# Performance work log

Hardware: AMD Instinct MI355X
Metric: run time of the kernel (lower is better)

## Reference

```python
import jax, jax.numpy as jnp
import numpy as np

CP_LEN = 256
FFT_SIZE = 1024
OFFSET = CP_LEN // 2                      # 128
PILOT_SPACING = 100
NSYMS = 824
TOTAL_SYMS = NSYMS + 1 + NSYMS // PILOT_SPACING   # 833
PAD_L = (FFT_SIZE - TOTAL_SYMS) // 2      # 95
PAD_R = FFT_SIZE - PAD_L - TOTAL_SYMS     # 96
PILOTS_IDX = np.arange(PAD_L, FFT_SIZE - PAD_R, PILOT_SPACING)  # 9 pilots

def _data_indices():
    # Statically unroll the original while-loop: gather all non-pilot data bins.
    idxs = []
    idx = 0
    jj = PAD_L + 1
    while idx < NSYMS:
        n = min(PILOT_SPACING - 1, NSYMS - idx)
        idxs.extend(range(jj, jj + n))
        idx += n
        jj += n + 1
    return np.asarray(idxs, dtype=np.int32)

DATA_IDX = _data_indices()  # [824]


def setup_inputs() -> dict:
    key = jax.random.key(0)
    # [batch, n_symbols, 2*(FFT_SIZE+CP_LEN)] interleaved I/Q floats
    in1 = jax.random.normal(key, (16, 1024, 2 * (FFT_SIZE + CP_LEN)), dtype=jnp.float32)
    return {"in1": in1}


def reference(in1):
    t = jnp.arange(FFT_SIZE, dtype=jnp.float32)
    # Deinterleave I/Q -> complex64
    iq = jax.lax.complex(in1[:, :, ::2], in1[:, :, 1::2])
    # FFT of the window starting at half the CP, then fftshift via roll
    spec = jnp.fft.fft(iq[:, :, OFFSET:OFFSET + FFT_SIZE], axis=2)
    result = jnp.roll(spec, FFT_SIZE // 2, axis=2)
    # Compensate timing-offset phase ramp
    result = result * jnp.exp(1j * OFFSET * t * (2.0 * np.pi / FFT_SIZE))
    # Estimate residual slope from pilot phase differences (wrapped to [-pi,pi])
    a = jnp.diff(jnp.angle(result[:, :, PILOTS_IDX]), axis=2)
    a = jnp.where(a > np.pi, a - 2.0 * np.pi, a)
    a = jnp.where(a < -np.pi, a + 2.0 * np.pi, a)
    mn = jnp.mean(a, axis=2)  # [B, S]
    result = result * jnp.exp(-1j * t * mn[:, :, None] / PILOT_SPACING)
    # Gather data (non-pilot) bins and interleave real/imag -> [B, S, 2*NSYMS]
    data = result[:, :, DATA_IDX]
    x = jnp.stack([data.real, data.imag], axis=-1).reshape(
        data.shape[0], data.shape[1], 2 * NSYMS)
    return x.astype(jnp.float32)
```

## Files before the change

kernel.cpp:

```cpp
#include <hip/hip_runtime.h>
#include <math.h>

#define NT      256
#define NSYMS   824
#define NPILOT  9

#define PADIDX(k) ((k) + ((k) >> 4))

#define C32_TWOPI_1024  6.1359233222901821136474609375e-3f

__device__ __forceinline__ float2 cmulf(float2 a, float2 b) {
    return make_float2(a.x * b.x - a.y * b.y, a.x * b.y + a.y * b.x);
}

template <int LM, int F>
__device__ __forceinline__ void dif_stage(float2* __restrict__ buf,
                                          const float2* __restrict__ W256,
                                          int i) {
    const int r = i & (LM - 1);
    const int base = ((i & ~(LM - 1)) << 2) | r;
    float2 a = buf[PADIDX(base)];
    float2 b = buf[PADIDX(base + LM)];
    float2 c = buf[PADIDX(base + 2 * LM)];
    float2 d = buf[PADIDX(base + 3 * LM)];
    float2 t0 = make_float2(a.x + c.x, a.y + c.y);
    float2 t1 = make_float2(a.x - c.x, a.y - c.y);
    float2 t2 = make_float2(b.x + d.x, b.y + d.y);
    float2 t3 = make_float2(b.x - d.x, b.y - d.y);
    float2 y0 = make_float2(t0.x + t2.x, t0.y + t2.y);
    float2 y1 = make_float2(t1.x + t3.y, t1.y - t3.x);
    float2 y2 = make_float2(t0.x - t2.x, t0.y - t2.y);
    float2 y3 = make_float2(t1.x - t3.y, t1.y + t3.x);
    const int e1 = F * r;
    const int e2 = 2 * F * r;
    const int e3 = 3 * F * r;
    float2 w1 = W256[PADIDX(e1)];
    float2 w2 = W256[PADIDX(e2 & 255)];
    if (e2 & 256) w2 = make_float2(w2.y, -w2.x);
    float2 w3 = W256[PADIDX(e3 & 255)];
    {
        const int q = e3 >> 8;
        if (q == 1)      w3 = make_float2(w3.y, -w3.x);
        else if (q == 2) w3 = make_float2(-w3.x, -w3.y);
    }
    buf[PADIDX(base)]          = y0;
    buf[PADIDX(base + LM)]     = cmulf(w1, y1);
    buf[PADIDX(base + 2 * LM)] = cmulf(w2, y2);
    buf[PADIDX(base + 3 * LM)] = cmulf(w3, y3);
}

__global__ void table_init(double2* __restrict__ Tg, float2* __restrict__ Wg) {
    const int t = threadIdx.x;
    double sn, cs;
    sincos((double)t * -6.1359231515425649189e-3, &sn, &cs);
    Tg[t] = make_double2(cs, sn);
    Wg[t] = make_float2((float)cs, (float)sn);
}

__global__ __launch_bounds__(NT, 8) void ofdm_kernel(const float* __restrict__ in,
                                                     float* __restrict__ out,
                                                     const double2* __restrict__ Tg,
                                                     const float2* __restrict__ Wg) {
    __shared__ double2 T256[256];
    __shared__ double2 u_s[NT];
    __shared__ float2  buf[1088];
    __shared__ float2  W256[272];
    __shared__ double2 pr2[NPILOT];
    __shared__ double  mn_s;

    const int row = blockIdx.x;
    const int tid = threadIdx.x;

    const float2* rin2 = (const float2*)(in + (size_t)row * 2560) + 128;
    float2 v0 = rin2[tid];
    float2 v1 = rin2[tid + 256];
    float2 v2 = rin2[tid + 512];
    float2 v3 = rin2[tid + 768];

    T256[tid] = Tg[tid];
    W256[PADIDX(tid)] = Wg[tid];

    double ux = ((double)v0.x - (double)v2.x) - ((double)v1.y - (double)v3.y);
    double uy = ((double)v0.y - (double)v2.y) + ((double)v1.x - (double)v3.x);

    {
        const int e2 = 2 * tid, e3 = 3 * tid;
        float2 w1 = Wg[tid];
        float2 w2 = Wg[e2 & 255];
        if (e2 & 256) w2 = make_float2(w2.y, -w2.x);
        float2 w3 = Wg[e3 & 255];
        {
            const int q = e3 >> 8;
            if (q == 1)      w3 = make_float2(w3.y, -w3.x);
            else if (q == 2) w3 = make_float2(-w3.x, -w3.y);
        }
        float2 t0 = make_float2(v0.x + v2.x, v0.y + v2.y);
        float2 t1 = make_float2(v0.x - v2.x, v0.y - v2.y);
        float2 t2 = make_float2(v1.x + v3.x, v1.y + v3.y);
        float2 t3 = make_float2(v1.x - v3.x, v1.y - v3.y);
        float2 y0 = make_float2(t0.x + t2.x, t0.y + t2.y);
        float2 y1 = make_float2(t1.x + t3.y, t1.y - t3.x);
        float2 y2 = make_float2(t0.x - t2.x, t0.y - t2.y);
        float2 y3 = make_float2(t1.x - t3.y, t1.y + t3.x);
        buf[PADIDX(tid)]       = y0;
        buf[PADIDX(tid + 256)] = cmulf(w1, y1);
        buf[PADIDX(tid + 512)] = cmulf(w2, y2);
        buf[PADIDX(tid + 768)] = cmulf(w3, y3);
    }
    u_s[tid] = make_double2(ux, uy);
    __syncthreads();

    if (tid < 16 * NPILOT) {
        const int p  = tid >> 4;
        const int g  = tid & 15;
        const int jj = 95 + 100 * p;
        const int K  = (jj + 512) & 1023;
        const double sc = (p & 1) ? -0.70710678118654752440
                                  :  0.70710678118654752440;
        int idx = (K * g) & 1023;
        const int step = (K * 16) & 1023;
        double2 acc = make_double2(0.0, 0.0);
        #pragma unroll
        for (int m = 0; m < 8; m++) {
            const int s = g + 16 * m;
            double2 u0 = u_s[s];
            double2 u1 = u_s[s + 128];
            double upx = u0.x + sc * (u1.x - u1.y);
            double upy = u0.y + sc * (u1.x + u1.y);
            double2 w  = T256[idx & 255];
            const int q = idx >> 8;
            double wx = w.x, wy = w.y;
            if (q & 1) { double t = wx; wx = wy; wy = -t; }
            if (q & 2) { wx = -wx; wy = -wy; }
            acc.x += wx * upx - wy * upy;
            acc.y += wx * upy + wy * upx;
            idx = (idx + step) & 1023;
        }
        #pragma unroll
        for (int off = 1; off < 16; off <<= 1) {
            acc.x += __shfl_xor(acc.x, off, 64);
            acc.y += __shfl_xor(acc.y, off, 64);
        }
        if (g == 0) pr2[p] = acc;
    }
    dif_stage<64, 4>(buf, W256, tid);
    __syncthreads();

    dif_stage<16, 16>(buf, W256, tid);
    if (tid >= 192) {
        const int p  = tid - 192;
        const int pc = (p < 8) ? p : 8;
        double2 acc = pr2[pc];
        const int jj = 95 + 100 * pc;
        float th32 = (float)(128 * jj) * C32_TWOPI_1024;
        double sn, cs;
        sincos((double)th32, &sn, &cs);
        double csf = (double)(float)cs;
        double snf = (double)(float)sn;
        double re = acc.x * csf - acc.y * snf;
        double im = acc.x * snf + acc.y * csf;
        double a  = atan2(im, re);
        double an = __shfl_down(a, 1, 64);
        double d  = an - a;
        if (d > 3.14159265358979323846)       d -= 6.28318530717958647693;
        else if (d < -3.14159265358979323846) d += 6.28318530717958647693;
        if (p >= 8) d = 0.0;
        d += __shfl_xor(d, 1, 64);
        d += __shfl_xor(d, 2, 64);
        d += __shfl_xor(d, 4, 64);
        if (p == 0) mn_s = d * 0.125;
    }
    __syncthreads();

    dif_stage<4, 64>(buf, W256, tid);
    __syncthreads();

    {
        const double mn001 = mn_s * 0.01;
        const int pb = PADIDX(4 * tid);
        float2 a = buf[pb];
        float2 b = buf[pb + 1];
        float2 c = buf[pb + 2];
        float2 d = buf[pb + 3];
        float2 t0 = make_float2(a.x + c.x, a.y + c.y);
        float2 t1 = make_float2(a.x - c.x, a.y - c.y);
        float2 t2 = make_float2(b.x + d.x, b.y + d.y);
        float2 t3 = make_float2(b.x - d.x, b.y - d.y);
        float2 y0 = make_float2(t0.x + t2.x, t0.y + t2.y);
        float2 y1 = make_float2(t1.x + t3.y, t1.y - t3.x);
        float2 y2 = make_float2(t0.x - t2.x, t0.y - t2.y);
        float2 y3 = make_float2(t1.x - t3.y, t1.y + t3.x);

        const int R = ((tid & 3) << 6) | (((tid >> 2) & 3) << 4) |
                      (((tid >> 4) & 3) << 2) | ((tid >> 6) & 3);

        float2* rout = (float2*)(out + (size_t)row * (2 * NSYMS));
        float2 ys[4] = { y2, y3, y0, y1 };
        #pragma unroll
        for (int k = 0; k < 4; k++) {
            const int jj = R + 256 * k;
            if (jj >= 96 && jj <= 927 && ((jj - 95) % 100) != 0) {
                const int dd = jj - 96 - (jj - 96) / 100;
                float2 z = ys[k];
                float th32 = (float)(128 * jj) * C32_TWOPI_1024;
                float ph = th32 - (float)(mn001 * (double)jj);
                float sn, cs;
                __sincosf(ph, &sn, &cs);
                rout[dd] = make_float2(z.x * cs - z.y * sn,
                                       z.x * sn + z.y * cs);
            }
        }
    }
}

extern "C" void kernel_launch(void* const* d_in, const int* in_sizes, int n_in,
                              void* d_out, int out_size, void* d_ws, size_t ws_size,
                              hipStream_t stream) {
    const float* in = (const float*)d_in[0];
    float* out = (float*)d_out;
    double2* Tg = (double2*)d_ws;
    float2*  Wg = (float2*)((char*)d_ws + 4096);
    table_init<<<dim3(1), dim3(256), 0, stream>>>(Tg, Wg);
    ofdm_kernel<<<dim3(16 * 1024), dim3(NT), 0, stream>>>(in, out, Tg, Wg);
}
```

Measured before the change: 268.5 us.

## Replace LDS radix-4 FFT stages with wavefront shuffle radix-2 butterflies

```diff
diff --git a/kernel.cpp b/kernel.cpp
--- a/kernel.cpp
+++ b/kernel.cpp
@@ -11,42 +11,6 @@
 
 __device__ __forceinline__ float2 cmulf(float2 a, float2 b) {
     return make_float2(a.x * b.x - a.y * b.y, a.x * b.y + a.y * b.x);
-}
-
-template <int LM, int F>
-__device__ __forceinline__ void dif_stage(float2* __restrict__ buf,
-                                          const float2* __restrict__ W256,
-                                          int i) {
-    const int r = i & (LM - 1);
-    const int base = ((i & ~(LM - 1)) << 2) | r;
-    float2 a = buf[PADIDX(base)];
-    float2 b = buf[PADIDX(base + LM)];
-    float2 c = buf[PADIDX(base + 2 * LM)];
-    float2 d = buf[PADIDX(base + 3 * LM)];
-    float2 t0 = make_float2(a.x + c.x, a.y + c.y);
-    float2 t1 = make_float2(a.x - c.x, a.y - c.y);
-    float2 t2 = make_float2(b.x + d.x, b.y + d.y);
-    float2 t3 = make_float2(b.x - d.x, b.y - d.y);
-    float2 y0 = make_float2(t0.x + t2.x, t0.y + t2.y);
-    float2 y1 = make_float2(t1.x + t3.y, t1.y - t3.x);
-    float2 y2 = make_float2(t0.x - t2.x, t0.y - t2.y);
-    float2 y3 = make_float2(t1.x - t3.y, t1.y + t3.x);
-    const int e1 = F * r;
-    const int e2 = 2 * F * r;
-    const int e3 = 3 * F * r;
-    float2 w1 = W256[PADIDX(e1)];
-    float2 w2 = W256[PADIDX(e2 & 255)];
-    if (e2 & 256) w2 = make_float2(w2.y, -w2.x);
-    float2 w3 = W256[PADIDX(e3 & 255)];
-    {
-        const int q = e3 >> 8;
-        if (q == 1)      w3 = make_float2(w3.y, -w3.x);
-        else if (q == 2) w3 = make_float2(-w3.x, -w3.y);
-    }
-    buf[PADIDX(base)]          = y0;
-    buf[PADIDX(base + LM)]     = cmulf(w1, y1);
-    buf[PADIDX(base + 2 * LM)] = cmulf(w2, y2);
-    buf[PADIDX(base + 3 * LM)] = cmulf(w3, y3);
 }
 
 __global__ void table_init(double2* __restrict__ Tg, float2* __restrict__ Wg) {
@@ -70,6 +34,8 @@
 
     const int row = blockIdx.x;
     const int tid = threadIdx.x;
+    const int b   = tid >> 6;
+    const int j   = tid & 63;
 
     const float2* rin2 = (const float2*)(in + (size_t)row * 2560) + 128;
     float2 v0 = rin2[tid];
@@ -113,8 +79,8 @@
     if (tid < 16 * NPILOT) {
         const int p  = tid >> 4;
         const int g  = tid & 15;
-        const int jj = 95 + 100 * p;
-        const int K  = (jj + 512) & 1023;
+        const int jp = 95 + 100 * p;
+        const int K  = (jp + 512) & 1023;
         const double sc = (p & 1) ? -0.70710678118654752440
                                   :  0.70710678118654752440;
         int idx = (K * g) & 1023;
@@ -143,16 +109,58 @@
         }
         if (g == 0) pr2[p] = acc;
     }
-    dif_stage<64, 4>(buf, W256, tid);
+
+    float2 x[4];
+    {
+        const int cb = 256 * b + j;
+        float2 a0 = buf[PADIDX(cb)];
+        float2 a1 = buf[PADIDX(cb + 64)];
+        float2 a2 = buf[PADIDX(cb + 128)];
+        float2 a3 = buf[PADIDX(cb + 192)];
+        float2 t0 = make_float2(a0.x + a2.x, a0.y + a2.y);
+        float2 t1 = make_float2(a0.x - a2.x, a0.y - a2.y);
+        float2 t2 = make_float2(a1.x + a3.x, a1.y + a3.y);
+        float2 t3 = make_float2(a1.x - a3.x, a1.y - a3.y);
+        float2 w1 = W256[PADIDX(4 * j)];
+        float2 w2 = W256[PADIDX((8 * j) & 255)];
+        if ((8 * j) & 256) w2 = make_float2(w2.y, -w2.x);
+        float2 w3 = W256[PADIDX((12 * j) & 255)];
+        {
+            const int q = (12 * j) >> 8;
+            if (q == 1)      w3 = make_float2(w3.y, -w3.x);
+            else if (q == 2) w3 = make_float2(-w3.x, -w3.y);
+        }
+        x[0] = make_float2(t0.x + t2.x, t0.y + t2.y);
+        x[1] = cmulf(w1, make_float2(t1.x + t3.y, t1.y - t3.x));
+        x[2] = cmulf(w2, make_float2(t0.x - t2.x, t0.y - t2.y));
+        x[3] = cmulf(w3, make_float2(t1.x - t3.y, t1.y + t3.x));
+    }
+    #pragma unroll
+    for (int st = 0; st < 6; st++) {
+        const int h = 32 >> st;
+        const int e = (16 << st) * (j & (h - 1));
+        float2 wh = make_float2(1.0f, 0.0f);
+        if (j & h) {
+            wh = W256[PADIDX(e & 255)];
+            if (e & 256) wh = make_float2(wh.y, -wh.x);
+        }
+        const float sg = (j & h) ? -1.0f : 1.0f;
+        #pragma unroll
+        for (int d = 0; d < 4; d++) {
+            float2 p = make_float2(__shfl_xor(x[d].x, h, 64),
+                                   __shfl_xor(x[d].y, h, 64));
+            float2 s = make_float2(p.x + sg * x[d].x, p.y + sg * x[d].y);
+            x[d] = cmulf(wh, s);
+        }
+    }
     __syncthreads();
 
-    dif_stage<16, 16>(buf, W256, tid);
     if (tid >= 192) {
         const int p  = tid - 192;
         const int pc = (p < 8) ? p : 8;
         double2 acc = pr2[pc];
-        const int jj = 95 + 100 * pc;
-        float th32 = (float)(128 * jj) * C32_TWOPI_1024;
+        const int jp = 95 + 100 * pc;
+        float th32 = (float)(128 * jp) * C32_TWOPI_1024;
         double sn, cs;
         sincos((double)th32, &sn, &cs);
         double csf = (double)(float)cs;
@@ -172,42 +180,23 @@
     }
     __syncthreads();
 
-    dif_stage<4, 64>(buf, W256, tid);
-    __syncthreads();
-
     {
         const double mn001 = mn_s * 0.01;
-        const int pb = PADIDX(4 * tid);
-        float2 a = buf[pb];
-        float2 b = buf[pb + 1];
-        float2 c = buf[pb + 2];
-        float2 d = buf[pb + 3];
-        float2 t0 = make_float2(a.x + c.x, a.y + c.y);
-        float2 t1 = make_float2(a.x - c.x, a.y - c.y);
-        float2 t2 = make_float2(b.x + d.x, b.y + d.y);
-        float2 t3 = make_float2(b.x - d.x, b.y - d.y);
-        float2 y0 = make_float2(t0.x + t2.x, t0.y + t2.y);
-        float2 y1 = make_float2(t1.x + t3.y, t1.y - t3.x);
-        float2 y2 = make_float2(t0.x - t2.x, t0.y - t2.y);
-        float2 y3 = make_float2(t1.x - t3.y, t1.y + t3.x);
-
-        const int R = ((tid & 3) << 6) | (((tid >> 2) & 3) << 4) |
-                      (((tid >> 4) & 3) << 2) | ((tid >> 6) & 3);
-
+        const int L = ((j & 1) << 5) | ((j & 2) << 3) | ((j & 4) << 1) |
+                      ((j & 8) >> 1) | ((j & 16) >> 3) | ((j & 32) >> 5);
         float2* rout = (float2*)(out + (size_t)row * (2 * NSYMS));
-        float2 ys[4] = { y2, y3, y0, y1 };
-        #pragma unroll
-        for (int k = 0; k < 4; k++) {
-            const int jj = R + 256 * k;
+        #pragma unroll
+        for (int d = 0; d < 4; d++) {
+            const int bin = (L << 4) + (d << 2) + b;
+            const int jj  = bin ^ 512;
             if (jj >= 96 && jj <= 927 && ((jj - 95) % 100) != 0) {
                 const int dd = jj - 96 - (jj - 96) / 100;
-                float2 z = ys[k];
                 float th32 = (float)(128 * jj) * C32_TWOPI_1024;
                 float ph = th32 - (float)(mn001 * (double)jj);
                 float sn, cs;
                 __sincosf(ph, &sn, &cs);
-                rout[dd] = make_float2(z.x * cs - z.y * sn,
-                                       z.x * sn + z.y * cs);
+                rout[dd] = make_float2(x[d].x * cs - x[d].y * sn,
+                                       x[d].x * sn + x[d].y * cs);
             }
         }
     }
```

New measurement: 307.0 us. 14.3% more time.

## Precompute twiddle and pilot rotation tables; drop shared double twiddle table

Applied to the files above, without the earlier changes.

```diff
diff --git a/kernel.cpp b/kernel.cpp
--- a/kernel.cpp
+++ b/kernel.cpp
@@ -49,19 +49,56 @@
     buf[PADIDX(base + 3 * LM)] = cmulf(w3, y3);
 }
 
-__global__ void table_init(double2* __restrict__ Tg, float2* __restrict__ Wg) {
+__global__ void table_init(double2* __restrict__ Tg,  float2* __restrict__ Wg,
+                           float2* __restrict__ W2g, float2* __restrict__ W3g,
+                           float2* __restrict__ S2w1, float2* __restrict__ S2w2,
+                           float2* __restrict__ S2w3, double2* __restrict__ Rg) {
     const int t = threadIdx.x;
     double sn, cs;
     sincos((double)t * -6.1359231515425649189e-3, &sn, &cs);
     Tg[t] = make_double2(cs, sn);
     Wg[t] = make_float2((float)cs, (float)sn);
+    __syncthreads();
+    {
+        float2 w2 = Wg[(2 * t) & 255];
+        if ((2 * t) & 256) w2 = make_float2(w2.y, -w2.x);
+        W2g[t] = w2;
+        float2 w3 = Wg[(3 * t) & 255];
+        const int q = (3 * t) >> 8;
+        if (q == 1)      w3 = make_float2(w3.y, -w3.x);
+        else if (q == 2) w3 = make_float2(-w3.x, -w3.y);
+        W3g[t] = w3;
+    }
+    if (t < 64) {
+        S2w1[t] = Wg[4 * t];
+        float2 a = Wg[(8 * t) & 255];
+        if ((8 * t) & 256) a = make_float2(a.y, -a.x);
+        S2w2[t] = a;
+        float2 b = Wg[(12 * t) & 255];
+        const int q = (12 * t) >> 8;
+        if (q == 1)      b = make_float2(b.y, -b.x);
+        else if (q == 2) b = make_float2(-b.x, -b.y);
+        S2w3[t] = b;
+    }
+    if (t < NPILOT) {
+        const int jj = 95 + 100 * t;
+        float th32 = (float)(128 * jj) * C32_TWOPI_1024;
+        double s2, c2;
+        sincos((double)th32, &s2, &c2);
+        Rg[t] = make_double2((double)(float)c2, (double)(float)s2);
+    }
 }
 
 __global__ __launch_bounds__(NT, 8) void ofdm_kernel(const float* __restrict__ in,
                                                      float* __restrict__ out,
                                                      const double2* __restrict__ Tg,
-                                                     const float2* __restrict__ Wg) {
-    __shared__ double2 T256[256];
+                                                     const float2* __restrict__ Wg,
+                                                     const float2* __restrict__ W2g,
+                                                     const float2* __restrict__ W3g,
+                                                     const float2* __restrict__ S2w1,
+                                                     const float2* __restrict__ S2w2,
+                                                     const float2* __restrict__ S2w3,
+                                                     const double2* __restrict__ Rg) {
     __shared__ double2 u_s[NT];
     __shared__ float2  buf[1088];
     __shared__ float2  W256[272];
@@ -77,23 +114,15 @@
     float2 v2 = rin2[tid + 512];
     float2 v3 = rin2[tid + 768];
 
-    T256[tid] = Tg[tid];
     W256[PADIDX(tid)] = Wg[tid];
 
     double ux = ((double)v0.x - (double)v2.x) - ((double)v1.y - (double)v3.y);
     double uy = ((double)v0.y - (double)v2.y) + ((double)v1.x - (double)v3.x);
 
     {
-        const int e2 = 2 * tid, e3 = 3 * tid;
         float2 w1 = Wg[tid];
-        float2 w2 = Wg[e2 & 255];
-        if (e2 & 256) w2 = make_float2(w2.y, -w2.x);
-        float2 w3 = Wg[e3 & 255];
-        {
-            const int q = e3 >> 8;
-            if (q == 1)      w3 = make_float2(w3.y, -w3.x);
-            else if (q == 2) w3 = make_float2(-w3.x, -w3.y);
-        }
+        float2 w2 = W2g[tid];
+        float2 w3 = W3g[tid];
         float2 t0 = make_float2(v0.x + v2.x, v0.y + v2.y);
         float2 t1 = make_float2(v0.x - v2.x, v0.y - v2.y);
         float2 t2 = make_float2(v1.x + v3.x, v1.y + v3.y);
@@ -113,12 +142,21 @@
     if (tid < 16 * NPILOT) {
         const int p  = tid >> 4;
         const int g  = tid & 15;
-        const int jj = 95 + 100 * p;
-        const int K  = (jj + 512) & 1023;
+        const int jp = 95 + 100 * p;
+        const int K  = (jp + 512) & 1023;
         const double sc = (p & 1) ? -0.70710678118654752440
                                   :  0.70710678118654752440;
-        int idx = (K * g) & 1023;
-        const int step = (K * 16) & 1023;
+        const int i0 = (K * g) & 1023;
+        const int is = (16 * K) & 1023;
+        double2 w0 = Tg[i0 & 255];
+        { const int q = i0 >> 8;
+          if (q & 1) { double tt = w0.x; w0.x = w0.y; w0.y = -tt; }
+          if (q & 2) { w0.x = -w0.x; w0.y = -w0.y; } }
+        double2 wsv = Tg[is & 255];
+        { const int q = is >> 8;
+          if (q & 1) { double tt = wsv.x; wsv.x = wsv.y; wsv.y = -tt; }
+          if (q & 2) { wsv.x = -wsv.x; wsv.y = -wsv.y; } }
+        double wx = w0.x, wy = w0.y;
         double2 acc = make_double2(0.0, 0.0);
         #pragma unroll
         for (int m = 0; m < 8; m++) {
@@ -127,14 +165,11 @@
             double2 u1 = u_s[s + 128];
             double upx = u0.x + sc * (u1.x - u1.y);
             double upy = u0.y + sc * (u1.x + u1.y);
-            double2 w  = T256[idx & 255];
-            const int q = idx >> 8;
-            double wx = w.x, wy = w.y;
-            if (q & 1) { double t = wx; wx = wy; wy = -t; }
-            if (q & 2) { wx = -wx; wy = -wy; }
             acc.x += wx * upx - wy * upy;
             acc.y += wx * upy + wy * upx;
-            idx = (idx + step) & 1023;
+            const double tw = wx * wsv.x - wy * wsv.y;
+            wy = wx * wsv.y + wy * wsv.x;
+            wx = tw;
         }
         #pragma unroll
         for (int off = 1; off < 16; off <<= 1) {
@@ -143,7 +178,30 @@
         }
         if (g == 0) pr2[p] = acc;
     }
-    dif_stage<64, 4>(buf, W256, tid);
+    {
+        const int r = tid & 63;
+        const int base = ((tid & ~63) << 2) | r;
+        const int pb = PADIDX(base);
+        float2 a = buf[pb];
+        float2 b = buf[pb + 68];
+        float2 c = buf[pb + 136];
+        float2 d = buf[pb + 204];
+        float2 w1 = S2w1[r];
+        float2 w2 = S2w2[r];
+        float2 w3 = S2w3[r];
+        float2 t0 = make_float2(a.x + c.x, a.y + c.y);
+        float2 t1 = make_float2(a.x - c.x, a.y - c.y);
+        float2 t2 = make_float2(b.x + d.x, b.y + d.y);
+        float2 t3 = make_float2(b.x - d.x, b.y - d.y);
+        float2 y0 = make_float2(t0.x + t2.x, t0.y + t2.y);
+        float2 y1 = make_float2(t1.x + t3.y, t1.y - t3.x);
+        float2 y2 = make_float2(t0.x - t2.x, t0.y - t2.y);
+        float2 y3 = make_float2(t1.x - t3.y, t1.y + t3.x);
+        buf[pb]       = y0;
+        buf[pb + 68]  = cmulf(w1, y1);
+        buf[pb + 136] = cmulf(w2, y2);
+        buf[pb + 204] = cmulf(w3, y3);
+    }
     __syncthreads();
 
     dif_stage<16, 16>(buf, W256, tid);
@@ -151,14 +209,9 @@
         const int p  = tid - 192;
         const int pc = (p < 8) ? p : 8;
         double2 acc = pr2[pc];
-        const int jj = 95 + 100 * pc;
-        float th32 = (float)(128 * jj) * C32_TWOPI_1024;
-        double sn, cs;
-        sincos((double)th32, &sn, &cs);
-        double csf = (double)(float)cs;
-        double snf = (double)(float)sn;
-        double re = acc.x * csf - acc.y * snf;
-        double im = acc.x * snf + acc.y * csf;
+        double2 rr  = Rg[pc];
+        double re = acc.x * rr.x - acc.y * rr.y;
+        double im = acc.x * rr.y + acc.y * rr.x;
         double a  = atan2(im, re);
         double an = __shfl_down(a, 1, 64);
         double d  = an - a;
@@ -218,8 +271,18 @@
                               hipStream_t stream) {
     const float* in = (const float*)d_in[0];
     float* out = (float*)d_out;
-    double2* Tg = (double2*)d_ws;
-    float2*  Wg = (float2*)((char*)d_ws + 4096);
-    table_init<<<dim3(1), dim3(256), 0, stream>>>(Tg, Wg);
-    ofdm_kernel<<<dim3(16 * 1024), dim3(NT), 0, stream>>>(in, out, Tg, Wg);
-}
+    char* ws = (char*)d_ws;
+    double2* Tg   = (double2*)(ws);
+    float2*  Wg   = (float2*) (ws + 4096);
+    float2*  W2g  = (float2*) (ws + 6144);
+    float2*  W3g  = (float2*) (ws + 8192);
+    float2*  S2w1 = (float2*) (ws + 10240);
+    float2*  S2w2 = (float2*) (ws + 10752);
+    float2*  S2w3 = (float2*) (ws + 11264);
+    double2* Rg   = (double2*)(ws + 11776);
+    table_init<<<dim3(1), dim3(256), 0, stream>>>(Tg, Wg, W2g, W3g,
+                                                  S2w1, S2w2, S2w3, Rg);
+    ofdm_kernel<<<dim3(16 * 1024), dim3(NT), 0, stream>>>(in, out, Tg, Wg,
+                                                          W2g, W3g,
+                                                          S2w1, S2w2, S2w3, Rg);
+}
```

Result: no change. 270.4 us (+0.7%).
